# Performance work log

Measured on AMD Instinct MI355X. Metric: run time of the kernel, lower is better.

## Reference

```python
import jax, jax.numpy as jnp
import numpy as np

B, C, IN_DIM, OUT_DIM, H = 8, 2048, 128, 128, 4
D = OUT_DIM // H  # d_k = 32


def setup_inputs() -> dict:
    key = jax.random.key(0)
    ks = jax.random.split(key, 7)
    s = 1.0 / np.sqrt(IN_DIM)
    x = jax.random.normal(ks[0], (B, C, IN_DIM), dtype=jnp.float32)
    adj = jax.random.uniform(ks[1], (B, C, C), dtype=jnp.float32)
    Wq = jax.random.uniform(ks[2], (IN_DIM, H * D), jnp.float32, -s, s)
    Wk = jax.random.uniform(ks[3], (IN_DIM, H * D), jnp.float32, -s, s)
    Wv = jax.random.uniform(ks[4], (IN_DIM, H * D), jnp.float32, -s, s)
    so = 1.0 / np.sqrt(H * D)
    Wo = jax.random.uniform(ks[5], (H * D, OUT_DIM), jnp.float32, -so, so)
    bo = jax.random.uniform(ks[6], (OUT_DIM,), jnp.float32, -so, so)
    return {"x": x, "adj": adj, "Wq": Wq, "Wk": Wk, "Wv": Wv, "Wo": Wo, "bo": bo}


def reference(x, adj, Wq, Wk, Wv, Wo, bo):
    # Project to per-head Q/K/V: (B, H, C, D)
    def proj(W):
        return (x @ W).reshape(B, C, H, D).transpose(0, 2, 1, 3)
    Q, K, V = proj(Wq), proj(Wk), proj(Wv)
    # Scaled dot-product scores, adjacency-gated, LeakyReLU(0.2), softmax
    scores = jnp.einsum('bhqd,bhkd->bhqk', Q, K) / jnp.sqrt(jnp.float32(D))
    scores = scores * adj[:, None, :, :]
    scores = jnp.where(scores > 0, scores, 0.2 * scores)  # LeakyReLU(0.2)
    attn = jax.nn.softmax(scores, axis=-1)  # dropout is identity at eval
    out = jnp.einsum('bhqk,bhkd->bhqd', attn, V)
    out = out.transpose(0, 2, 1, 3).reshape(B, C, H * D)  # concat heads
    return out @ Wo + bo
```

## Files before the change

### kernel.cpp

```cpp
#include <hip/hip_runtime.h>
#include <hip/hip_bf16.h>

constexpr int B_  = 8;
constexpr int C_  = 2048;
constexpr int IND = 128;
constexpr int H_  = 4;
constexpr int D_  = 32;
constexpr int M_  = B_ * C_;
constexpr float QSCALE = 0.17677669529663687f;
constexpr float L2E    = 1.4426950408889634f;
constexpr float QL2    = QSCALE * L2E;

constexpr int KSPLIT = 4;
constexpr int KPG = C_ / KSPLIT;

typedef __attribute__((ext_vector_type(8))) short short8;
typedef __attribute__((ext_vector_type(4))) short s4t;
typedef __attribute__((ext_vector_type(4))) float f4t;
typedef __attribute__((ext_vector_type(4))) unsigned short us4;

#if __has_builtin(__builtin_amdgcn_mfma_f32_16x16x16bf16_1k)
#define MFMA16(a, b, c) __builtin_amdgcn_mfma_f32_16x16x16bf16_1k(a, b, c, 0, 0, 0)
#else
#define MFMA16(a, b, c) (c)
#endif
#define MFMA32(a, b, c) __builtin_amdgcn_mfma_f32_16x16x32_bf16(a, b, c, 0, 0, 0)

__device__ __forceinline__ unsigned short f2bf(float f) {
    union { float f; unsigned u; } v; v.f = f;
    unsigned u = v.u + 0x7fffu + ((v.u >> 16) & 1u);
    return (unsigned short)(u >> 16);
}

__device__ __forceinline__ s4t pack4_bf16(float p0, float p1, float p2, float p3) {
#if __has_builtin(__builtin_amdgcn_cvt_pk_bf16_f32)
    auto a = __builtin_amdgcn_cvt_pk_bf16_f32(p0, p1);
    auto b = __builtin_amdgcn_cvt_pk_bf16_f32(p2, p3);
    unsigned u[2];
    __builtin_memcpy(&u[0], &a, 4);
    __builtin_memcpy(&u[1], &b, 4);
    s4t pp;
    __builtin_memcpy(&pp, u, 8);
    return pp;
#else
    s4t pp;
    pp[0] = (short)f2bf(p0); pp[1] = (short)f2bf(p1);
    pp[2] = (short)f2bf(p2); pp[3] = (short)f2bf(p3);
    return pp;
#endif
}

__device__ __forceinline__ short8 cvt8(float4 a, float4 b) {
    s4t x = pack4_bf16(a.x, a.y, a.z, a.w);
    s4t y = pack4_bf16(b.x, b.y, b.z, b.w);
    short8 r;
    r[0] = x[0]; r[1] = x[1]; r[2] = x[2]; r[3] = x[3];
    r[4] = y[0]; r[5] = y[1]; r[6] = y[2]; r[7] = y[3];
    return r;
}

__global__ __launch_bounds__(256) void prep_w_kernel(
    const float* __restrict__ Wq, const float* __restrict__ Wk,
    const float* __restrict__ Wv, const float* __restrict__ Wo,
    unsigned short* __restrict__ Wtb)
{
    __shared__ unsigned short lds[16][130];
    const int t  = threadIdx.x;
    const int n0 = blockIdx.x * 16;

    const float* src; int nb; float sc = 1.0f;
    if      (n0 < 128) { src = Wq; nb = n0;       sc = QL2; }
    else if (n0 < 256) { src = Wk; nb = n0 - 128; }
    else if (n0 < 384) { src = Wv; nb = n0 - 256; }
    else               { src = Wo; nb = n0 - 384; }

    const int nn = t & 15, kk = t >> 4;
#pragma unroll
    for (int kb = 0; kb < 8; ++kb) {
        const int k = kb * 16 + kk;
        lds[nn][k] = f2bf(src[k * IND + nb + nn] * sc);
    }
    __syncthreads();
    const int k = t & 127, rr = t >> 7;
#pragma unroll
    for (int it = 0; it < 8; ++it) {
        const int r = it * 2 + rr;
        Wtb[(size_t)(n0 + r) * IND + k] = lds[r][k];
    }
}

__global__ __launch_bounds__(192) void qkv_proj_kernel(
    const float* __restrict__ x, const unsigned short* __restrict__ Wtb,
    unsigned short* __restrict__ Qb, unsigned short* __restrict__ Kb,
    unsigned short* __restrict__ Vt)
{
    const int t = threadIdx.x;
    const int w = t >> 6;
    const int l = t & 63;
    const int lo = l & 15, hi = l >> 4;
    const int tok0 = blockIdx.x * 16;
    const int b  = tok0 >> 11;
    const int cb = tok0 & 2047;
    const int tile0 = blockIdx.y * 4;

    short8 xb[4];
    const float* xrow = x + (size_t)(tok0 + lo) * IND;
#pragma unroll
    for (int kc = 0; kc < 4; ++kc) {
        const float4 a = *(const float4*)(xrow + kc * 32 + hi * 8);
        const float4 c = *(const float4*)(xrow + kc * 32 + hi * 8 + 4);
        xb[kc] = cvt8(a, c);
    }

    const unsigned short* wbase = Wtb + (size_t)(w * 128) * IND;
#pragma unroll
    for (int tile = 0; tile < 4; ++tile) {
        const int n0 = (tile0 + tile) * 16;
        short8 wf[4];
#pragma unroll
        for (int kc = 0; kc < 4; ++kc)
            wf[kc] = *(const short8*)(wbase + (size_t)(n0 + lo) * IND +
                                      kc * 32 + hi * 8);
        f4t acc = 0.f;
        if (w < 2) {
#pragma unroll
            for (int kc = 0; kc < 4; ++kc) acc = MFMA32(wf[kc], xb[kc], acc);
            us4 v;
#pragma unroll
            for (int r = 0; r < 4; ++r) v[r] = f2bf(acc[r]);
            unsigned short* O = (w == 0) ? Qb : Kb;
            *(us4*)(O + (size_t)(tok0 + lo) * IND + n0 + hi * 4) = v;
        } else {
#pragma unroll
            for (int kc = 0; kc < 4; ++kc) acc = MFMA32(xb[kc], wf[kc], acc);
            us4 v;
#pragma unroll
            for (int r = 0; r < 4; ++r) v[r] = f2bf(acc[r]);
            *(us4*)(Vt + ((size_t)(b * IND) + n0 + lo) * C_ + cb + hi * 4) = v;
        }
    }
}

__global__ __launch_bounds__(256, 4) void attn_kernel(
    const unsigned short* __restrict__ Qb, const unsigned short* __restrict__ Kb,
    const unsigned short* __restrict__ Vt, const float* __restrict__ adj,
    float* __restrict__ Opart, float* __restrict__ lpart)
{
    __shared__ __align__(16) char Ksm[2][4096];
    __shared__ __align__(16) char Vsm[2][4096];
    __shared__ __align__(16) char Asm[2][4096];

    const int t  = threadIdx.x;
    const int s  = t >> 6;
    const int l  = t & 63;
    const int lo = l & 15, hi = l >> 4;
    const int b  = blockIdx.y;
    const int kz = blockIdx.z;
    const int q0 = blockIdx.x * 64;
    const int qs = q0 + s * 16 + lo;
    const int kzoff = kz * KPG;
    const int NCH = KPG / 16;

    const int keyS = s * 4 + (l >> 4);
    const char* srcK = (const char*)Kb + ((size_t)(b * C_ + kzoff) + keyS) * 256
                       + (((l & 15) * 16) ^ ((keyS & 7) << 4));
    const int dS = s * 32 + (l >> 1);
    const char* srcV = (const char*)Vt + (size_t)(b * IND + dS) * (C_ * 2)
                       + (size_t)kzoff * 2 + (l & 1) * 16;
    const int qS = s * 16 + (l >> 2);
    const char* srcA = (const char*)adj
                       + ((size_t)(b * C_ + q0 + qS) * C_ + kzoff) * 4
                       + (l & 3) * 16;

#if __has_builtin(__builtin_amdgcn_global_load_lds)
#define GLL(gp, lp) __builtin_amdgcn_global_load_lds( \
    (const __attribute__((address_space(1))) unsigned int*)(gp), \
    (__attribute__((address_space(3))) unsigned int*)(lp), 16, 0, 0)
#else
#define GLL(gp, lp) (void)(gp)
#endif

    auto stage = [&](int c, int buf) {
        GLL(srcK + (size_t)c * 4096, Ksm[buf] + s * 1024);
        GLL(srcV + (size_t)c * 32,   Vsm[buf] + s * 1024);
        GLL(srcA + (size_t)c * 64,   Asm[buf] + s * 1024);
    };

    short8 qf[4];
#pragma unroll
    for (int h = 0; h < 4; ++h)
        qf[h] = *(const short8*)(Qb + ((size_t)(b * C_) + qs) * IND + h * 32 + hi * 8);
    __builtin_amdgcn_sched_barrier(0);
    stage(0, 0);
    __builtin_amdgcn_sched_barrier(0);
    stage(1, 1);
    __builtin_amdgcn_sched_barrier(0);

    f4t acc[4][2];
#pragma unroll
    for (int h = 0; h < 4; ++h) { acc[h][0] = 0.f; acc[h][1] = 0.f; }
    float ls[4] = {0.f, 0.f, 0.f, 0.f};

    const int x7 = (lo & 7) << 4;

    auto computeC = [&](int buf) {
        const char* Kl = Ksm[buf];
        const char* Vl = Vsm[buf];
        const char* Al = Asm[buf];
        short8 kf[4];
#pragma unroll
        for (int h = 0; h < 4; ++h)
            kf[h] = *(const short8*)(Kl + lo * 256 + ((h * 64 + hi * 16) ^ x7));
        s4t vf[8];
#pragma unroll
        for (int h = 0; h < 4; ++h) {
            vf[h * 2]     = *(const s4t*)(Vl + (h * 32 + lo) * 32 + hi * 8);
            vf[h * 2 + 1] = *(const s4t*)(Vl + (h * 32 + 16 + lo) * 32 + hi * 8);
        }
        const f4t av = *(const f4t*)(Al + (s * 16 + lo) * 64 + hi * 16);
#pragma unroll
        for (int h = 0; h < 4; ++h) {
            f4t st4 = MFMA32(kf[h], qf[h], (f4t)0.f);
            float p[4];
#pragma unroll
            for (int r = 0; r < 4; ++r) {
                const float a = st4[r] * av[r];
                const float m = fmaxf(a, 0.2f * a);
                p[r] = exp2f(m);
                ls[h] += p[r];
            }
            const s4t pp = pack4_bf16(p[0], p[1], p[2], p[3]);
            acc[h][0] = MFMA16(pp, vf[h * 2], acc[h][0]);
            acc[h][1] = MFMA16(pp, vf[h * 2 + 1], acc[h][1]);
        }
    };

    for (int c = 0; c < NCH; ++c) {
        if (c + 1 < NCH) { asm volatile("s_waitcnt vmcnt(3)" ::: "memory"); }
        else             { asm volatile("s_waitcnt vmcnt(0)" ::: "memory"); }
        __builtin_amdgcn_sched_barrier(0);
        __builtin_amdgcn_s_barrier();
        __builtin_amdgcn_sched_barrier(0);

        computeC(c & 1);

        asm volatile("s_waitcnt lgkmcnt(0)" ::: "memory");
        __builtin_amdgcn_sched_barrier(0);
        __builtin_amdgcn_s_barrier();
        __builtin_amdgcn_sched_barrier(0);
        if (c + 2 < NCH) stage(c + 2, c & 1);
    }

#pragma unroll
    for (int h = 0; h < 4; ++h) {
        ls[h] += __shfl_xor(ls[h], 16, 64);
        ls[h] += __shfl_xor(ls[h], 32, 64);
    }

    const size_t BHC   = (size_t)B_ * H_ * C_;
    const size_t obase = (size_t)kz * BHC;

    const float lw = (hi == 0) ? ls[0] : (hi == 1) ? ls[1] : (hi == 2) ? ls[2] : ls[3];
    lpart[obase + (size_t)(b * H_ + hi) * C_ + qs] = lw;

#pragma unroll
    for (int h = 0; h < 4; ++h) {
        const size_t rb = obase + (size_t)(b * H_ + h) * C_ + q0 + s * 16 + hi * 4;
#pragma unroll
        for (int dh = 0; dh < 2; ++dh)
#pragma unroll
            for (int r = 0; r < 4; ++r)
                Opart[(rb + r) * D_ + dh * 16 + lo] = acc[h][dh][r];
    }
#undef GLL
}

__global__ __launch_bounds__(256) void combine_kernel(
    const float* __restrict__ Opart, const float* __restrict__ lpart,
    unsigned short* __restrict__ AOb)
{
    const int cid = blockIdx.x * 256 + threadIdx.x;
    const int j   = cid & 7;
    const int idx = cid >> 3;
    const int q  = idx & (C_ - 1);
    const int bh = idx >> 11;
    const int h  = bh & (H_ - 1);
    const int b  = bh >> 2;
    const size_t BHC = (size_t)B_ * H_ * C_;

    float4 acc = {0.f, 0.f, 0.f, 0.f};
    float lsum = 0.f;
#pragma unroll
    for (int kz = 0; kz < KSPLIT; ++kz) {
        const size_t base = (size_t)kz * BHC + idx;
        lsum += lpart[base];
        const float4 v = *(const float4*)(Opart + base * D_ + j * 4);
        acc.x += v.x; acc.y += v.y; acc.z += v.z; acc.w += v.w;
    }
    const float inv = 1.f / lsum;
    us4 o;
    o[0] = f2bf(acc.x * inv); o[1] = f2bf(acc.y * inv);
    o[2] = f2bf(acc.z * inv); o[3] = f2bf(acc.w * inv);
    *(us4*)(AOb + ((size_t)(b * C_) + q) * IND + h * D_ + j * 4) = o;
}

__global__ __launch_bounds__(256) void out_proj_kernel(
    const unsigned short* __restrict__ AOb, const unsigned short* __restrict__ Wtb,
    const float* __restrict__ bo, float* __restrict__ out)
{
    const int t  = threadIdx.x;
    const int w  = t >> 6;
    const int l  = t & 63;
    const int lo = l & 15, hi = l >> 4;
    const int tok0 = blockIdx.x * 16;

    short8 af[4];
    const unsigned short* arow = AOb + (size_t)(tok0 + lo) * IND;
#pragma unroll
    for (int kc = 0; kc < 4; ++kc)
        af[kc] = *(const short8*)(arow + kc * 32 + hi * 8);

    const unsigned short* wbase = Wtb + (size_t)384 * IND;
#pragma unroll
    for (int tt = 0; tt < 2; ++tt) {
        const int n0 = w * 32 + tt * 16;
        short8 wf[4];
#pragma unroll
        for (int kc = 0; kc < 4; ++kc)
            wf[kc] = *(const short8*)(wbase + (size_t)(n0 + lo) * IND +
                                      kc * 32 + hi * 8);
        f4t acc = 0.f;
#pragma unroll
        for (int kc = 0; kc < 4; ++kc) acc = MFMA32(wf[kc], af[kc], acc);
        const f4t bv = *(const f4t*)(bo + n0 + hi * 4);
        float4 o;
        o.x = acc[0] + bv[0]; o.y = acc[1] + bv[1];
        o.z = acc[2] + bv[2]; o.w = acc[3] + bv[3];
        *(float4*)(out + (size_t)(tok0 + lo) * IND + n0 + hi * 4) = o;
    }
}

extern "C" void kernel_launch(void* const* d_in, const int* in_sizes, int n_in,
                              void* d_out, int out_size, void* d_ws, size_t ws_size,
                              hipStream_t stream) {
    const float* x   = (const float*)d_in[0];
    const float* adj = (const float*)d_in[1];
    const float* Wq  = (const float*)d_in[2];
    const float* Wk  = (const float*)d_in[3];
    const float* Wv  = (const float*)d_in[4];
    const float* Wo  = (const float*)d_in[5];
    const float* bo  = (const float*)d_in[6];
    float* out = (float*)d_out;

    unsigned short* Wtb = (unsigned short*)d_ws;
    unsigned short* Qb  = Wtb + (size_t)512 * IND;
    unsigned short* Kb  = Qb + (size_t)M_ * IND;
    unsigned short* Vt  = Kb + (size_t)M_ * IND;
    unsigned short* AOb = Vt + (size_t)M_ * IND;
    float* Opart = (float*)(AOb + (size_t)M_ * IND);
    float* lpart = Opart + (size_t)KSPLIT * B_ * H_ * C_ * D_;

    hipLaunchKernelGGL(prep_w_kernel, dim3(32), dim3(256), 0, stream,
                       Wq, Wk, Wv, Wo, Wtb);
    hipLaunchKernelGGL(qkv_proj_kernel, dim3(M_ / 16, 2), dim3(192), 0, stream,
                       x, Wtb, Qb, Kb, Vt);
    hipLaunchKernelGGL(attn_kernel, dim3(C_ / 64, B_, KSPLIT), dim3(256), 0, stream,
                       Qb, Kb, Vt, adj, Opart, lpart);
    hipLaunchKernelGGL(combine_kernel, dim3(B_ * H_ * C_ * 8 / 256), dim3(256), 0, stream,
                       Opart, lpart, AOb);
    hipLaunchKernelGGL(out_proj_kernel, dim3(M_ / 16), dim3(256), 0, stream,
                       AOb, Wtb, bo, out);
}
```

Measured before the change: 286.5 us.

## Triple-buffer attention staging and fuse split-K combine into output projection

The attention loop moves from double to triple LDS buffering, so the next stage is issued before compute and the second barrier per chunk is dropped. The combine kernel is folded into the output projection, which now sums the split-K partials, normalizes them and writes bf16 tiles to swizzled LDS before the MFMA. This removes one kernel launch and the round trip of the AO intermediate through global memory. The cost is 50% more LDS per attention block, which may lower occupancy, and a tighter buffer-reuse ordering that leans on the single remaining barrier.

```diff
diff --git a/kernel.cpp b/kernel.cpp
--- a/kernel.cpp
+++ b/kernel.cpp
@@ -146,9 +146,9 @@
     const unsigned short* __restrict__ Vt, const float* __restrict__ adj,
     float* __restrict__ Opart, float* __restrict__ lpart)
 {
-    __shared__ __align__(16) char Ksm[2][4096];
-    __shared__ __align__(16) char Vsm[2][4096];
-    __shared__ __align__(16) char Asm[2][4096];
+    __shared__ __align__(16) char Ksm[3][4096];
+    __shared__ __align__(16) char Vsm[3][4096];
+    __shared__ __align__(16) char Asm[3][4096];
 
     const int t  = threadIdx.x;
     const int s  = t >> 6;
@@ -235,6 +235,7 @@
         }
     };
 
+    int bc = 0, bn = 1, bs = 2;
     for (int c = 0; c < NCH; ++c) {
         if (c + 1 < NCH) { asm volatile("s_waitcnt vmcnt(3)" ::: "memory"); }
         else             { asm volatile("s_waitcnt vmcnt(0)" ::: "memory"); }
@@ -242,13 +243,10 @@
         __builtin_amdgcn_s_barrier();
         __builtin_amdgcn_sched_barrier(0);
 
-        computeC(c & 1);
-
-        asm volatile("s_waitcnt lgkmcnt(0)" ::: "memory");
-        __builtin_amdgcn_sched_barrier(0);
-        __builtin_amdgcn_s_barrier();
-        __builtin_amdgcn_sched_barrier(0);
-        if (c + 2 < NCH) stage(c + 2, c & 1);
+        if (c + 2 < NCH) stage(c + 2, bs);
+        computeC(bc);
+
+        const int tmp = bc; bc = bn; bn = bs; bs = tmp;
     }
 
 #pragma unroll
@@ -275,50 +273,52 @@
 #undef GLL
 }
 
-__global__ __launch_bounds__(256) void combine_kernel(
+__global__ __launch_bounds__(256) void out_proj_kernel(
     const float* __restrict__ Opart, const float* __restrict__ lpart,
-    unsigned short* __restrict__ AOb)
+    const unsigned short* __restrict__ Wtb, const float* __restrict__ bo,
+    float* __restrict__ out)
 {
-    const int cid = blockIdx.x * 256 + threadIdx.x;
-    const int j   = cid & 7;
-    const int idx = cid >> 3;
-    const int q  = idx & (C_ - 1);
-    const int bh = idx >> 11;
-    const int h  = bh & (H_ - 1);
-    const int b  = bh >> 2;
-    const size_t BHC = (size_t)B_ * H_ * C_;
-
-    float4 acc = {0.f, 0.f, 0.f, 0.f};
-    float lsum = 0.f;
-#pragma unroll
-    for (int kz = 0; kz < KSPLIT; ++kz) {
-        const size_t base = (size_t)kz * BHC + idx;
-        lsum += lpart[base];
-        const float4 v = *(const float4*)(Opart + base * D_ + j * 4);
-        acc.x += v.x; acc.y += v.y; acc.z += v.z; acc.w += v.w;
-    }
-    const float inv = 1.f / lsum;
-    us4 o;
-    o[0] = f2bf(acc.x * inv); o[1] = f2bf(acc.y * inv);
-    o[2] = f2bf(acc.z * inv); o[3] = f2bf(acc.w * inv);
-    *(us4*)(AOb + ((size_t)(b * C_) + q) * IND + h * D_ + j * 4) = o;
-}
-
-__global__ __launch_bounds__(256) void out_proj_kernel(
-    const unsigned short* __restrict__ AOb, const unsigned short* __restrict__ Wtb,
-    const float* __restrict__ bo, float* __restrict__ out)
-{
+    __shared__ __align__(16) char AOsm[4096];
+
     const int t  = threadIdx.x;
     const int w  = t >> 6;
     const int l  = t & 63;
     const int lo = l & 15, hi = l >> 4;
     const int tok0 = blockIdx.x * 16;
+    const int b  = tok0 >> 11;
+    const int q0 = tok0 & 2047;
+    const size_t BHC = (size_t)B_ * H_ * C_;
+
+    {
+        const int ra = l >> 3;
+        const int dq = l & 7;
+        float4 va = {0.f, 0.f, 0.f, 0.f}, vb = {0.f, 0.f, 0.f, 0.f};
+        float la = 0.f, lb = 0.f;
+#pragma unroll
+        for (int kz = 0; kz < KSPLIT; ++kz) {
+            const size_t rowb = (size_t)kz * BHC + (size_t)(b * H_ + w) * C_ + q0;
+            la += lpart[rowb + ra];
+            lb += lpart[rowb + ra + 8];
+            const float* R = Opart + rowb * D_;
+            const float4 u = *(const float4*)(R + l * 4);
+            const float4 v = *(const float4*)(R + 256 + l * 4);
+            va.x += u.x; va.y += u.y; va.z += u.z; va.w += u.w;
+            vb.x += v.x; vb.y += v.y; vb.z += v.z; vb.w += v.w;
+        }
+        const float ia = 1.f / la, ib = 1.f / lb;
+        const s4t pa = pack4_bf16(va.x * ia, va.y * ia, va.z * ia, va.w * ia);
+        const s4t pb = pack4_bf16(vb.x * ib, vb.y * ib, vb.z * ib, vb.w * ib);
+        const int colb = w * 64 + dq * 8;
+        *(s4t*)(AOsm + ra * 256       + (colb ^ ((ra & 7) << 4))) = pa;
+        *(s4t*)(AOsm + (ra + 8) * 256 + (colb ^ ((ra & 7) << 4))) = pb;
+    }
+    __syncthreads();
 
     short8 af[4];
-    const unsigned short* arow = AOb + (size_t)(tok0 + lo) * IND;
 #pragma unroll
     for (int kc = 0; kc < 4; ++kc)
-        af[kc] = *(const short8*)(arow + kc * 32 + hi * 8);
+        af[kc] = *(const short8*)(AOsm + lo * 256 +
+                                  ((kc * 64 + hi * 16) ^ ((lo & 7) << 4)));
 
     const unsigned short* wbase = Wtb + (size_t)384 * IND;
 #pragma unroll
@@ -366,8 +366,6 @@
                        x, Wtb, Qb, Kb, Vt);
     hipLaunchKernelGGL(attn_kernel, dim3(C_ / 64, B_, KSPLIT), dim3(256), 0, stream,
                        Qb, Kb, Vt, adj, Opart, lpart);
-    hipLaunchKernelGGL(combine_kernel, dim3(B_ * H_ * C_ * 8 / 256), dim3(256), 0, stream,
-                       Opart, lpart, AOb);
     hipLaunchKernelGGL(out_proj_kernel, dim3(M_ / 16), dim3(256), 0, stream,
-                       AOb, Wtb, bo, out);
-}
+                       Opart, lpart, Wtb, bo, out);
+}
```

Result: no change. 285.5 us (-0.3%).
